# Performance work log

Measured on AMD Instinct MI355X. Metric: run time of the kernel, lower is better.

## Reference

```python
import jax, jax.numpy as jnp
import numpy as np

BINS = 256

def _conv_x(t, k):
    # t: [N,1,H,W], k: [3] tap filter along width, 'same' padding
    return jax.lax.conv_general_dilated(t, k.reshape(1, 1, 1, 3), (1, 1), [(0, 0), (1, 1)])

def _conv_y(t, k):
    # t: [N,1,H,W], k: [3] tap filter along height, 'same' padding
    return jax.lax.conv_general_dilated(t, k.reshape(1, 1, 3, 1), (1, 1), [(1, 1), (0, 0)])

def calc_invCR(x):
    # Vectorized equivalent of the per-slice torch.histc loop:
    # 256-bin histogram over [-1,1] per (batch*channel) slice, Shannon entropy in bits / 8.
    n, _, h, w = x.shape
    res = h * w
    xf = x.reshape(n, res)
    valid = ((xf >= -1.0) & (xf <= 1.0)).astype(jnp.float32)
    # bin index; value exactly == max (1.0) falls into the last bin, matching torch.histc
    bins = jnp.clip(jnp.floor((xf + 1.0) * (BINS / 2.0)), 0, BINS - 1).astype(jnp.int32)
    counts = jnp.zeros((n, BINS), jnp.float32).at[jnp.arange(n)[:, None], bins].add(valid)
    p = counts / res
    ent = jnp.sum(jnp.where(p > 0, -p * jnp.log2(jnp.where(p > 0, p, 1.0)), 0.0))
    return ent / (8.0 * n)

def _forward(x, px, ux, cx, rx, py, uy, cy, ry):
    b, c, h, w = x.shape
    img = x.reshape(b * c, 1, h, w)
    cur = img
    xos, yos = [], []
    for lvl in range(5):
        xe, xo = cur[:, :, :, ::2], cur[:, :, :, 1::2]
        xo = xo - _conv_x(xe, px)
        xe = xe + _conv_x(xo, ux)
        xo = xo - _conv_x(xe, cx)
        xe = xe + _conv_x(xo, rx)
        ye, yo = xe[:, :, ::2, :], xe[:, :, 1::2, :]
        yo = yo - _conv_y(ye, py)
        if lvl < 2:
            ye = ye + _conv_y(yo, uy)
        # levels 3-5 in the source apply update_y to the (discarded) x?e tensor
        # (`x3e = x3e + self.update_y(x3o)`); that result is never used, so it is a
        # no-op for the output and is faithfully omitted here.
        yo = yo - _conv_y(ye, cy)
        ye = ye + _conv_y(yo, ry)
        xos.append(xo)
        yos.append(yo)
        cur = ye
    out = cur
    for xo, yo in zip(reversed(xos), reversed(yos)):
        out = jnp.concatenate((jnp.concatenate((out, yo), axis=2), xo), axis=3)
    deltas = jnp.fmod(out + 1.0, 2.0) - 1.0  # wrap residuals into [-1,1]
    loss1 = 255.0 * jnp.sqrt(jnp.mean(jnp.square(deltas)))
    loss0 = 255.0 * jnp.sqrt(jnp.mean(jnp.square(img)))
    invCR0 = calc_invCR(img)
    invCR1 = calc_invCR(deltas)
    return loss1, loss0, invCR0, invCR1

def setup_inputs() -> dict:
    key = jax.random.key(0)
    ks = jax.random.split(key, 9)
    inp = {"x": jax.random.uniform(ks[0], (32, 3, 512, 512), jnp.float32)}
    for i, name in enumerate(["px", "ux", "cx", "rx", "py", "uy", "cy", "ry"]):
        inp[name] = 0.25 * jax.random.normal(ks[i + 1], (3,), jnp.float32)
    return inp

def reference(x, px, ux, cx, rx, py, uy, cy, ry):
    return _forward(x, px, ux, cx, rx, py, uy, cy, ry)
```

## Files before the change

### kernel.cpp

```cpp
#include <hip/hip_runtime.h>
#include <math.h>

#define NIMG 96
#define NSLOT 1024
#define RES_INV (1.0f / 262144.0f)

__device__ __forceinline__ float wrap1(float v) {
  float t = v + 1.0f;
  return t - 2.0f * truncf(t * 0.5f) - 1.0f;
}
__device__ __forceinline__ int bin_fast(float v) {
  int b = (int)fmaf(v, 128.0f, 128.0f);
  return (b > 255) ? 255 : b;
}

template<int P, int SEGP, int USE_UY, int DO_IMG>
__global__ void __launch_bounds__(256) klift_fused(
    const float* __restrict__ src, float* __restrict__ ye_out,
    const float* __restrict__ kpx, const float* __restrict__ kux,
    const float* __restrict__ kcx, const float* __restrict__ krx,
    const float* __restrict__ kpy, const float* __restrict__ kuy,
    const float* __restrict__ kcy, const float* __restrict__ kry,
    double* __restrict__ partial,
    unsigned* __restrict__ hist_img, unsigned* __restrict__ hist_delta)
{
  constexpr int W2 = 64 * P;
  constexpr int H2 = W2;
  constexpr int H  = 2 * H2;
  constexpr int NP = SEGP + 8;
  constexpr int NR = 2 * NP;
  constexpr int NITER = NR / 4;
  __shared__ float tile[NR][W2];
  __shared__ unsigned shd[256];
  __shared__ unsigned shi[256];

  const int t = threadIdx.x, w = t >> 6, lane = t & 63;
  const int img = blockIdx.y;
  const int R0 = blockIdx.x * SEGP;
  const int base_in = 2 * R0 - 8;

  shd[t] = 0;
  if (DO_IMG) shi[t] = 0;
  __syncthreads();

  const float px0 = kpx[0], px1 = kpx[1], px2 = kpx[2];
  const float ux0 = kux[0], ux1 = kux[1], ux2 = kux[2];
  const float cx0 = kcx[0], cx1 = kcx[1], cx2 = kcx[2];
  const float rx0 = krx[0], rx1 = krx[1], rx2 = krx[2];
  const float py0 = kpy[0], py1 = kpy[1], py2 = kpy[2];
  const float uy0 = kuy[0], uy1 = kuy[1], uy2 = kuy[2];
  const float cy0 = kcy[0], cy1 = kcy[1], cy2 = kcy[2];
  const float ry0 = kry[0], ry1 = kry[1], ry2 = kry[2];

  const float* ip = src + (size_t)img * H * (2 * W2);
  float sqi = 0.f, sqd = 0.f;

  auto stepm = [&](float (&d)[P], float (&s)[P], float k0, float k1, float k2, float sgn) {
    float L = __shfl_up(s[P - 1], 1); if (lane == 0) L = 0.f;
    float R = __shfl_down(s[0], 1);   if (lane == 63) R = 0.f;
    float prev = L;
#pragma unroll
    for (int j = 0; j < P; j++) {
      float nxt = (j == P - 1) ? R : s[(j + 1) < P ? (j + 1) : 0];
      d[j] += sgn * (k0 * prev + k1 * s[j] + k2 * nxt);
      prev = s[j];
    }
  };
  auto ldrow = [&](int lr, float4& A, float4& B, bool chk) {
    const int gin = base_in + lr;
    if (!chk || ((unsigned)gin < (unsigned)H)) {
      const float* rp = ip + (size_t)gin * (2 * W2) + lane * (2 * P);
      if (P == 1) { float2 v = *(const float2*)rp; A.x = v.x; A.y = v.y; }
      else {
        A = *(const float4*)rp;
        if (P == 4) B = *(const float4*)(rp + 4);
      }
    } else {
      A = make_float4(0.f, 0.f, 0.f, 0.f);
      B = make_float4(0.f, 0.f, 0.f, 0.f);
    }
  };

  const int wcol = (P == 4) ? ((lane ^ ((lane >> 3) & 7)) * 4)
                 : (P == 2) ? (lane * 2) : lane;

  float4 cA = make_float4(0.f,0.f,0.f,0.f), cB = cA, nA = cA, nB = cA;
  ldrow(w, cA, cB, true);
#pragma unroll
  for (int i = 0; i < NITER; ++i) {
    const int lr = w + 4 * i;
    if (i + 1 < NITER)
      ldrow(lr + 4, nA, nB, (i + 1 < 2) || (i + 1 >= NITER - 2));
    const bool owned = (i >= 2) && (i < NITER - 2);
    float e[P], o[P];
    e[0] = cA.x; o[0] = cA.y;
    if (P >= 2) { e[P > 1 ? 1 : 0] = cA.z; o[P > 1 ? 1 : 0] = cA.w; }
    if (P == 4) {
      e[P > 2 ? 2 : 0] = cB.x; o[P > 2 ? 2 : 0] = cB.y;
      e[P > 3 ? 3 : 0] = cB.z; o[P > 3 ? 3 : 0] = cB.w;
    }
    if (DO_IMG && owned) {
#pragma unroll
      for (int j = 0; j < P; j++) {
        sqi += e[j] * e[j] + o[j] * o[j];
        atomicAdd(&shi[bin_fast(e[j])], 1u);
        atomicAdd(&shi[bin_fast(o[j])], 1u);
      }
    }
    stepm(o, e, px0, px1, px2, -1.f);
    stepm(e, o, ux0, ux1, ux2,  1.f);
    stepm(o, e, cx0, cx1, cx2, -1.f);
    stepm(e, o, rx0, rx1, rx2,  1.f);
    if (P == 4) {
      *(float4*)&tile[lr][wcol] =
          make_float4(e[0], e[P > 1 ? 1 : 0], e[P > 2 ? 2 : 0], e[P > 3 ? 3 : 0]);
    } else if (P == 2) {
      *(float2*)&tile[lr][wcol] = make_float2(e[0], e[P > 1 ? 1 : 0]);
    } else {
      tile[lr][wcol] = e[0];
    }
    if (owned) {
#pragma unroll
      for (int j = 0; j < P; j++) {
        float d = wrap1(o[j]);
        sqd += d * d;
        atomicAdd(&shd[bin_fast(d)], 1u);
      }
    }
    cA = nA; cB = nB;
  }
  __syncthreads();

  {
    constexpr int NSP = 256 / W2;
    constexpr int LEN = SEGP / NSP;
    constexpr int WIN = LEN + 8;
    const int col = t % W2;
    const int half = t / W2;
    const int q0 = half * LEN;
    int colr;
    if (P == 4) {
      const int ch = (col >> 2) ^ ((col >> 5) & 7);
      colr = (ch << 2) | (col & 3);
    } else colr = col;

    float ee[WIN], oo[WIN];
#pragma unroll
    for (int q = 0; q < WIN; ++q) {
      ee[q] = tile[2 * (q0 + q)][colr];
      oo[q] = tile[2 * (q0 + q) + 1][colr];
    }
#pragma unroll
    for (int q = 0; q < WIN; ++q) {
      float U = (q > 0) ? ee[q - 1] : 0.f;
      float D = (q < WIN - 1) ? ee[q + 1] : 0.f;
      oo[q] -= py0 * U + py1 * ee[q] + py2 * D;
    }
    if (USE_UY) {
#pragma unroll
      for (int q = 0; q < WIN; ++q) {
        float U = (q > 0) ? oo[q - 1] : 0.f;
        float D = (q < WIN - 1) ? oo[q + 1] : 0.f;
        ee[q] += uy0 * U + uy1 * oo[q] + uy2 * D;
      }
    }
#pragma unroll
    for (int q = 0; q < WIN; ++q) {
      float U = (q > 0) ? ee[q - 1] : 0.f;
      float D = (q < WIN - 1) ? ee[q + 1] : 0.f;
      oo[q] -= cy0 * U + cy1 * ee[q] + cy2 * D;
    }
#pragma unroll
    for (int q = 0; q < WIN; ++q) {
      float U = (q > 0) ? oo[q - 1] : 0.f;
      float D = (q < WIN - 1) ? oo[q + 1] : 0.f;
      ee[q] += ry0 * U + ry1 * oo[q] + ry2 * D;
    }
    float* outp = ye_out + (size_t)img * H2 * W2 + col;
#pragma unroll
    for (int q = 4; q < 4 + LEN; ++q) {
      const int g = R0 + q0 + q - 4;
      float d = wrap1(oo[q]);
      sqd += d * d;
      atomicAdd(&shd[bin_fast(d)], 1u);
      outp[(size_t)g * W2] = ee[q];
    }
  }

  for (int off = 32; off; off >>= 1) {
    sqd += __shfl_down(sqd, off);
    if (DO_IMG) sqi += __shfl_down(sqi, off);
  }
  if (lane == 0) {
    const int bid = blockIdx.x + blockIdx.y * gridDim.x;
    const int slot = (bid * 4 + w) & (NSLOT - 1);
    atomicAdd(&partial[NSLOT + slot], (double)sqd);
    if (DO_IMG) atomicAdd(&partial[slot], (double)sqi);
  }
  __syncthreads();
  unsigned hd = shd[t];
  if (hd) atomicAdd(&hist_delta[img * 256 + t], hd);
  if (DO_IMG) {
    unsigned hi = shi[t];
    if (hi) atomicAdd(&hist_img[img * 256 + t], hi);
  }
}

__global__ void __launch_bounds__(256) klift_tail64(
    const float* __restrict__ src,
    const float* __restrict__ kpx, const float* __restrict__ kux,
    const float* __restrict__ kcx, const float* __restrict__ krx,
    const float* __restrict__ kpy, const float* __restrict__ kcy,
    const float* __restrict__ kry,
    double* __restrict__ partial, unsigned* __restrict__ hist_delta)
{
  __shared__ float tile[64][65];
  __shared__ unsigned shd[256];
  const int t = threadIdx.x;
  const int img = blockIdx.x;
  shd[t] = 0;

  const float* sp = src + (size_t)img * 64 * 64;
  for (int idx = t; idx < 64 * 16; idx += 256) {
    const int r = idx >> 4, c4 = (idx & 15) << 2;
    float4 v = *(const float4*)(sp + r * 64 + c4);
    tile[r][c4] = v.x; tile[r][c4 + 1] = v.y;
    tile[r][c4 + 2] = v.z; tile[r][c4 + 3] = v.w;
  }
  const float px0 = kpx[0], px1 = kpx[1], px2 = kpx[2];
  const float ux0 = kux[0], ux1 = kux[1], ux2 = kux[2];
  const float cx0 = kcx[0], cx1 = kcx[1], cx2 = kcx[2];
  const float rx0 = krx[0], rx1 = krx[1], rx2 = krx[2];
  const float pc0 = kpy[0] + kcy[0], pc1 = kpy[1] + kcy[1], pc2 = kpy[2] + kcy[2];
  const float ry0 = kry[0], ry1 = kry[1], ry2 = kry[2];
  float sqd = 0.f;
  __syncthreads();

  for (int l = 0; l < 2; ++l) {
    const int s = 1 << l, n = 64 >> l, half = n >> 1;
    const int totx = n * half;

    for (int idx = t; idx < totx; idx += 256) {
      const int r = (idx / half) * s, c = idx % half;
      float L = (c > 0) ? tile[r][(2 * c - 2) * s] : 0.f;
      float M = tile[r][2 * c * s];
      float R = (c < half - 1) ? tile[r][(2 * c + 2) * s] : 0.f;
      tile[r][(2 * c + 1) * s] -= px0 * L + px1 * M + px2 * R;
    }
    __syncthreads();
    for (int idx = t; idx < totx; idx += 256) {
      const int r = (idx / half) * s, c = idx % half;
      float L = (c > 0) ? tile[r][(2 * c - 1) * s] : 0.f;
      float M = tile[r][(2 * c + 1) * s];
      float R = (c < half - 1) ? tile[r][(2 * c + 3) * s] : 0.f;
      tile[r][2 * c * s] += ux0 * L + ux1 * M + ux2 * R;
    }
    __syncthreads();
    for (int idx = t; idx < totx; idx += 256) {
      const int r = (idx / half) * s, c = idx % half;
      float L = (c > 0) ? tile[r][(2 * c - 2) * s] : 0.f;
      float M = tile[r][2 * c * s];
      float R = (c < half - 1) ? tile[r][(2 * c + 2) * s] : 0.f;
      tile[r][(2 * c + 1) * s] -= cx0 * L + cx1 * M + cx2 * R;
    }
    __syncthreads();
    for (int idx = t; idx < totx; idx += 256) {
      const int r = (idx / half) * s, c = idx % half;
      float L = (c > 0) ? tile[r][(2 * c - 1) * s] : 0.f;
      float M = tile[r][(2 * c + 1) * s];
      float R = (c < half - 1) ? tile[r][(2 * c + 3) * s] : 0.f;
      tile[r][2 * c * s] += rx0 * L + rx1 * M + rx2 * R;
    }
    __syncthreads();
    for (int idx = t; idx < totx; idx += 256) {
      const int r = (idx / half) * s, c = idx % half;
      float d = wrap1(tile[r][(2 * c + 1) * s]);
      sqd += d * d;
      atomicAdd(&shd[bin_fast(d)], 1u);
    }
    const int toty = half * half;
    for (int idx = t; idx < toty; idx += 256) {
      const int r = idx / half, j = idx % half, col = j * 2 * s;
      float U = (r > 0) ? tile[(2 * r - 2) * s][col] : 0.f;
      float M = tile[(2 * r) * s][col];
      float D = (r < half - 1) ? tile[(2 * r + 2) * s][col] : 0.f;
      tile[(2 * r + 1) * s][col] -= pc0 * U + pc1 * M + pc2 * D;
    }
    __syncthreads();
    for (int idx = t; idx < toty; idx += 256) {
      const int r = idx / half, j = idx % half, col = j * 2 * s;
      float U = (r > 0) ? tile[(2 * r - 1) * s][col] : 0.f;
      float M = tile[(2 * r + 1) * s][col];
      float D = (r < half - 1) ? tile[(2 * r + 3) * s][col] : 0.f;
      tile[(2 * r) * s][col] += ry0 * U + ry1 * M + ry2 * D;
    }
    __syncthreads();
    for (int idx = t; idx < toty; idx += 256) {
      const int r = idx / half, j = idx % half, col = j * 2 * s;
      float d = wrap1(tile[(2 * r + 1) * s][col]);
      sqd += d * d;
      atomicAdd(&shd[bin_fast(d)], 1u);
      if (l == 1) {
        float d2 = wrap1(tile[(2 * r) * s][col]);
        sqd += d2 * d2;
        atomicAdd(&shd[bin_fast(d2)], 1u);
      }
    }
    __syncthreads();
  }

  for (int off = 32; off; off >>= 1) sqd += __shfl_down(sqd, off);
  __shared__ float swv[4];
  if ((t & 63) == 0) swv[t >> 6] = sqd;
  __syncthreads();
  if (t == 0) {
    double tot = (double)swv[0] + swv[1] + swv[2] + swv[3];
    atomicAdd(&partial[NSLOT + (img & (NSLOT - 1))], tot);
  }
  unsigned hd = shd[t];
  if (hd) atomicAdd(&hist_delta[img * 256 + t], hd);
}

__global__ void __launch_bounds__(256) kfinal(
    const double* __restrict__ partial,
    const unsigned* __restrict__ hist_img,
    const unsigned* __restrict__ hist_delta,
    float* __restrict__ out)
{
  __shared__ double sI[256], sD[256], sPi[256], sPd[256];
  const int t = threadIdx.x;
  double entI = 0.0, entD = 0.0;
  for (int img = 0; img < NIMG; ++img) {
    unsigned ci = hist_img[img * 256 + t];
    if (ci) { float p = (float)ci * RES_INV; entI += (double)(-p * log2f(p)); }
    unsigned cd = hist_delta[img * 256 + t];
    if (cd) { float p = (float)cd * RES_INV; entD += (double)(-p * log2f(p)); }
  }
  double pi = 0.0, pd = 0.0;
  for (int s = t; s < NSLOT; s += 256) {
    pi += partial[s];
    pd += partial[NSLOT + s];
  }
  sI[t] = entI; sD[t] = entD; sPi[t] = pi; sPd[t] = pd;
  __syncthreads();
  for (int s = 128; s; s >>= 1) {
    if (t < s) {
      sI[t] += sI[t + s]; sD[t] += sD[t + s];
      sPi[t] += sPi[t + s]; sPd[t] += sPd[t + s];
    }
    __syncthreads();
  }
  if (t == 0) {
    const double tot = (double)NIMG * 262144.0;
    out[0] = (float)(255.0 * sqrt(sPd[0] / tot));
    out[1] = (float)(255.0 * sqrt(sPi[0] / tot));
    out[2] = (float)(sI[0] / (8.0 * NIMG));
    out[3] = (float)(sD[0] / (8.0 * NIMG));
  }
}

extern "C" void kernel_launch(void* const* d_in, const int* in_sizes, int n_in,
                              void* d_out, int out_size, void* d_ws, size_t ws_size,
                              hipStream_t stream)
{
  const float* x  = (const float*)d_in[0];
  const float* px = (const float*)d_in[1];
  const float* ux = (const float*)d_in[2];
  const float* cx = (const float*)d_in[3];
  const float* rx = (const float*)d_in[4];
  const float* py = (const float*)d_in[5];
  const float* uy = (const float*)d_in[6];
  const float* cy = (const float*)d_in[7];
  const float* ry = (const float*)d_in[8];
  float* out = (float*)d_out;

  char* ws = (char*)d_ws;
  double*   partial    = (double*)ws;
  unsigned* hist_img   = (unsigned*)(ws + 2 * NSLOT * 8);
  unsigned* hist_delta = (unsigned*)(ws + 2 * NSLOT * 8 + NIMG * 256 * 4);
  float* buf0 = (float*)(ws + (1 << 20));
  float* buf1 = (float*)(ws + (1 << 20) + ((size_t)32 << 20));
  float* buf2 = (float*)(ws + (1 << 20) + ((size_t)40 << 20));

  hipMemsetAsync(ws, 0, 2 * NSLOT * 8 + 2 * NIMG * 256 * 4, stream);

  klift_fused<4, 16, 1, 1><<<dim3(16, NIMG), 256, 0, stream>>>(
      x, buf0, px, ux, cx, rx, py, uy, cy, ry, partial, hist_img, hist_delta);
  klift_fused<2, 8, 1, 0><<<dim3(16, NIMG), 256, 0, stream>>>(
      buf0, buf1, px, ux, cx, rx, py, uy, cy, ry, partial, hist_img, hist_delta);
  klift_fused<1, 8, 0, 0><<<dim3(8, NIMG), 256, 0, stream>>>(
      buf1, buf2, px, ux, cx, rx, py, uy, cy, ry, partial, hist_img, hist_delta);
  klift_tail64<<<NIMG, 256, 0, stream>>>(buf2, px, ux, cx, rx, py, cy, ry,
                                         partial, hist_delta);
  kfinal<<<1, 256, 0, stream>>>(partial, hist_img, hist_delta, out);
}
```

Measured before the change: 89.26 us.

## Privatize shared histograms per wave pair, use explicit FMAs, halve first-level segment

Splits each block's shared-memory histograms into two copies chosen by wave pair, which cuts contention on the LDS atomics, and sums the copies at flush time. The lifting stencil arithmetic is rewritten as chains of fused multiply-adds with the signs folded into the coefficients, removing the separate sign multiply. The first-level kernel now uses 8-row segments on twice as many blocks. That gives more parallelism but adds halo recomputation, since each block still processes 8 extra halo rows.

```diff
diff --git a/kernel.cpp b/kernel.cpp
--- a/kernel.cpp
+++ b/kernel.cpp
@@ -31,16 +31,17 @@
   constexpr int NR = 2 * NP;
   constexpr int NITER = NR / 4;
   __shared__ float tile[NR][W2];
-  __shared__ unsigned shd[256];
-  __shared__ unsigned shi[256];
+  __shared__ unsigned shd[2][256];
+  __shared__ unsigned shi[2][256];
 
   const int t = threadIdx.x, w = t >> 6, lane = t & 63;
+  const int hsel = w >> 1;
   const int img = blockIdx.y;
   const int R0 = blockIdx.x * SEGP;
   const int base_in = 2 * R0 - 8;
 
-  shd[t] = 0;
-  if (DO_IMG) shi[t] = 0;
+  shd[0][t] = 0; shd[1][t] = 0;
+  if (DO_IMG) { shi[0][t] = 0; shi[1][t] = 0; }
   __syncthreads();
 
   const float px0 = kpx[0], px1 = kpx[1], px2 = kpx[2];
@@ -55,14 +56,14 @@
   const float* ip = src + (size_t)img * H * (2 * W2);
   float sqi = 0.f, sqd = 0.f;
 
-  auto stepm = [&](float (&d)[P], float (&s)[P], float k0, float k1, float k2, float sgn) {
+  auto stepm = [&](float (&d)[P], float (&s)[P], float k0, float k1, float k2) {
     float L = __shfl_up(s[P - 1], 1); if (lane == 0) L = 0.f;
     float R = __shfl_down(s[0], 1);   if (lane == 63) R = 0.f;
     float prev = L;
 #pragma unroll
     for (int j = 0; j < P; j++) {
       float nxt = (j == P - 1) ? R : s[(j + 1) < P ? (j + 1) : 0];
-      d[j] += sgn * (k0 * prev + k1 * s[j] + k2 * nxt);
+      d[j] = fmaf(k0, prev, fmaf(k1, s[j], fmaf(k2, nxt, d[j])));
       prev = s[j];
     }
   };
@@ -103,14 +104,14 @@
 #pragma unroll
       for (int j = 0; j < P; j++) {
         sqi += e[j] * e[j] + o[j] * o[j];
-        atomicAdd(&shi[bin_fast(e[j])], 1u);
-        atomicAdd(&shi[bin_fast(o[j])], 1u);
-      }
-    }
-    stepm(o, e, px0, px1, px2, -1.f);
-    stepm(e, o, ux0, ux1, ux2,  1.f);
-    stepm(o, e, cx0, cx1, cx2, -1.f);
-    stepm(e, o, rx0, rx1, rx2,  1.f);
+        atomicAdd(&shi[hsel][bin_fast(e[j])], 1u);
+        atomicAdd(&shi[hsel][bin_fast(o[j])], 1u);
+      }
+    }
+    stepm(o, e, -px0, -px1, -px2);
+    stepm(e, o,  ux0,  ux1,  ux2);
+    stepm(o, e, -cx0, -cx1, -cx2);
+    stepm(e, o,  rx0,  rx1,  rx2);
     if (P == 4) {
       *(float4*)&tile[lr][wcol] =
           make_float4(e[0], e[P > 1 ? 1 : 0], e[P > 2 ? 2 : 0], e[P > 3 ? 3 : 0]);
@@ -124,7 +125,7 @@
       for (int j = 0; j < P; j++) {
         float d = wrap1(o[j]);
         sqd += d * d;
-        atomicAdd(&shd[bin_fast(d)], 1u);
+        atomicAdd(&shd[hsel][bin_fast(d)], 1u);
       }
     }
     cA = nA; cB = nB;
@@ -154,27 +155,27 @@
     for (int q = 0; q < WIN; ++q) {
       float U = (q > 0) ? ee[q - 1] : 0.f;
       float D = (q < WIN - 1) ? ee[q + 1] : 0.f;
-      oo[q] -= py0 * U + py1 * ee[q] + py2 * D;
+      oo[q] = fmaf(-py0, U, fmaf(-py1, ee[q], fmaf(-py2, D, oo[q])));
     }
     if (USE_UY) {
 #pragma unroll
       for (int q = 0; q < WIN; ++q) {
         float U = (q > 0) ? oo[q - 1] : 0.f;
         float D = (q < WIN - 1) ? oo[q + 1] : 0.f;
-        ee[q] += uy0 * U + uy1 * oo[q] + uy2 * D;
+        ee[q] = fmaf(uy0, U, fmaf(uy1, oo[q], fmaf(uy2, D, ee[q])));
       }
     }
 #pragma unroll
     for (int q = 0; q < WIN; ++q) {
       float U = (q > 0) ? ee[q - 1] : 0.f;
       float D = (q < WIN - 1) ? ee[q + 1] : 0.f;
-      oo[q] -= cy0 * U + cy1 * ee[q] + cy2 * D;
+      oo[q] = fmaf(-cy0, U, fmaf(-cy1, ee[q], fmaf(-cy2, D, oo[q])));
     }
 #pragma unroll
     for (int q = 0; q < WIN; ++q) {
       float U = (q > 0) ? oo[q - 1] : 0.f;
       float D = (q < WIN - 1) ? oo[q + 1] : 0.f;
-      ee[q] += ry0 * U + ry1 * oo[q] + ry2 * D;
+      ee[q] = fmaf(ry0, U, fmaf(ry1, oo[q], fmaf(ry2, D, ee[q])));
     }
     float* outp = ye_out + (size_t)img * H2 * W2 + col;
 #pragma unroll
@@ -182,7 +183,7 @@
       const int g = R0 + q0 + q - 4;
       float d = wrap1(oo[q]);
       sqd += d * d;
-      atomicAdd(&shd[bin_fast(d)], 1u);
+      atomicAdd(&shd[hsel][bin_fast(d)], 1u);
       outp[(size_t)g * W2] = ee[q];
     }
   }
@@ -198,10 +199,10 @@
     if (DO_IMG) atomicAdd(&partial[slot], (double)sqi);
   }
   __syncthreads();
-  unsigned hd = shd[t];
+  unsigned hd = shd[0][t] + shd[1][t];
   if (hd) atomicAdd(&hist_delta[img * 256 + t], hd);
   if (DO_IMG) {
-    unsigned hi = shi[t];
+    unsigned hi = shi[0][t] + shi[1][t];
     if (hi) atomicAdd(&hist_img[img * 256 + t], hi);
   }
 }
@@ -384,7 +385,7 @@
 
   hipMemsetAsync(ws, 0, 2 * NSLOT * 8 + 2 * NIMG * 256 * 4, stream);
 
-  klift_fused<4, 16, 1, 1><<<dim3(16, NIMG), 256, 0, stream>>>(
+  klift_fused<4, 8, 1, 1><<<dim3(32, NIMG), 256, 0, stream>>>(
       x, buf0, px, ux, cx, rx, py, uy, cy, ry, partial, hist_img, hist_delta);
   klift_fused<2, 8, 1, 0><<<dim3(16, NIMG), 256, 0, stream>>>(
       buf0, buf1, px, ux, cx, rx, py, uy, cy, ry, partial, hist_img, hist_delta);
```

Measured after the change: 89.30 us, median of 2. No clear change (+0.0%).
